# Kernel tuning notes

Measured on AMD Instinct MI355X. Metric: run time of the kernel, lower is better.

## Reference

```python
import jax, jax.numpy as jnp
import numpy as np

B = 524288
N_BUNDLES = 8
BUNDLE_DIM = 16
TOTAL_DIM = N_BUNDLES * BUNDLE_DIM  # 128
HIDDEN = 64
EPS = 1e-8


def setup_inputs() -> dict:
    key = jax.random.key(0)
    ks = jax.random.split(key, 8)
    z = jax.random.normal(ks[0], (B, TOTAL_DIM), dtype=jnp.float32)
    # norm MLP: Linear(n_bundles->hidden), GELU, Linear(hidden->hidden), GELU, Linear(hidden->n_bundles, no bias)
    W1 = jax.random.normal(ks[1], (HIDDEN, N_BUNDLES), dtype=jnp.float32) * (1.0 / np.sqrt(N_BUNDLES))
    b1 = jax.random.normal(ks[2], (HIDDEN,), dtype=jnp.float32) * 0.01
    W2 = jax.random.normal(ks[3], (HIDDEN, HIDDEN), dtype=jnp.float32) * (1.0 / np.sqrt(HIDDEN))
    b2 = jax.random.normal(ks[4], (HIDDEN,), dtype=jnp.float32) * 0.01
    W3 = jax.random.normal(ks[5], (N_BUNDLES, HIDDEN), dtype=jnp.float32) * (1.0 / np.sqrt(HIDDEN))
    # mixing_weights[i][j]: [d_i, d_j], init randn*0.01 -> stacked [n, n, d, d]
    mixW = jax.random.normal(ks[6], (N_BUNDLES, N_BUNDLES, BUNDLE_DIM, BUNDLE_DIM), dtype=jnp.float32) * 0.01
    gate_bias = jnp.zeros((N_BUNDLES,), dtype=jnp.float32)
    return {"z": z, "W1": W1, "b1": b1, "W2": W2, "b2": b2, "W3": W3,
            "mixW": mixW, "gate_bias": gate_bias}


def reference(z, W1, b1, W2, b2, W3, mixW, gate_bias):
    Bsz = z.shape[0]
    zb = z.reshape(Bsz, N_BUNDLES, BUNDLE_DIM)            # [B, n, d]
    # per-bundle norms (+eps as in torch source)
    norms = jnp.linalg.norm(zb, axis=-1) + EPS            # [B, n]
    # norm MLP with exact GELU (torch default), softplus scale
    h = jax.nn.gelu(norms @ W1.T + b1, approximate=False)
    h = jax.nn.gelu(h @ W2.T + b2, approximate=False)
    scales = jax.nn.softplus(h @ W3.T)                    # [B, n]
    equiv = zb * scales[:, :, None]                       # [B, n, d]
    # mixed_i = sum_j bundles_j @ W_ij^T ; mixW[i,j] is [d_out_i, d_in_j]
    mixed = jnp.einsum('bjk,ijdk->bid', zb, mixW)         # [B, n, d]
    gates = jax.nn.sigmoid(gate_bias)                     # [n]
    combined = equiv + gates[None, :, None] * mixed       # [B, n, d]
    return z + combined.reshape(Bsz, TOTAL_DIM)
```

## Files before the change

### kernel.cpp

```cpp
#include <hip/hip_runtime.h>
#include <hip/hip_bf16.h>

constexpr int NB  = 8;
constexpr int TD  = 128;
constexpr int HID = 64;
constexpr int ROWS = 128;

typedef __attribute__((ext_vector_type(8))) short bf16x8;
typedef __attribute__((ext_vector_type(4))) float f32x4;

union U { unsigned u[4]; bf16x8 v; };

__device__ __forceinline__ unsigned int pk2(float a, float b) {
    __hip_bfloat162 h = __float22bfloat162_rn(float2{a, b});
    unsigned int u; __builtin_memcpy(&u, &h, 4); return u;
}

__device__ __forceinline__ float gelu_fast(float x) {
    const float u = x * 0.70710678118f;
    const float a = fabsf(u);
    const float t = __builtin_amdgcn_rcpf(fmaf(0.3275911f, a, 1.0f));
    float p = fmaf(t, 1.061405429f, -1.453152027f);
    p = fmaf(t, p, 1.421413741f);
    p = fmaf(t, p, -0.284496736f);
    p = fmaf(t, p, 0.254829592f);
    p = p * t;
    const float e  = __builtin_amdgcn_exp2f(-a * a * 1.44269504f);
    const float pe = p * e;
    const float s  = (u >= 0.f) ? (2.0f - pe) : pe;
    return 0.5f * x * s;
}

constexpr size_t WS_NEED_BYTES = 10752 * 4;

__global__ __launch_bounds__(256, 1)
void cvt_weights(const float* __restrict__ W1, const float* __restrict__ W2,
                 const float* __restrict__ W3, const float* __restrict__ mixW,
                 unsigned* __restrict__ ws)
{
    const int t = threadIdx.x;
#pragma unroll
    for (int i = 0; i < 32; ++i) {
        const int p = t + i * 256;
        const int o = 2 * p;
        const int c = o >> 7, f = o & 127;
        const int ii = c >> 4, d = c & 15, j = f >> 4, k = f & 15;
        const float2 v = *(const float2*)(mixW + ii * 2048 + j * 256 + d * 16 + k);
        ws[p] = pk2(v.x, v.y);
    }
#pragma unroll
    for (int i = 0; i < 8; ++i) {
        const int p = t + i * 256;
        const float2 v = *(const float2*)(W2 + 2 * p);
        ws[8192 + p] = pk2(v.x, v.y);
    }
    {
        const float2 v1 = *(const float2*)(W1 + 2 * t);
        ws[10240 + t] = pk2(v1.x, v1.y);
        const float2 v3 = *(const float2*)(W3 + 2 * t);
        ws[10496 + t] = pk2(v3.x, v3.y);
    }
}

template<bool USE_WS>
__global__ __launch_bounds__(256, 4)
void soft_equiv(const float* __restrict__ z,  const float* __restrict__ W1,
                const float* __restrict__ b1, const float* __restrict__ W2,
                const float* __restrict__ b2, const float* __restrict__ W3,
                const float* __restrict__ mixW, const float* __restrict__ gb,
                const unsigned short* __restrict__ wsu,
                float* __restrict__ out)
{
    __shared__ __align__(16) unsigned short zs[ROWS * TD];
    __shared__ __align__(16) unsigned short hn[ROWS * NB];
    __shared__ float sca[ROWS * 9];

    const int t    = threadIdx.x;
    const int lane = t & 63;
    const int w    = t >> 6;
    const int hi   = lane >> 4;
    const int lo   = lane & 15;
    const size_t row0 = (size_t)blockIdx.x * ROWS;
    const float* ztile = z + row0 * TD;
    const f32x4 z4 = {0.f, 0.f, 0.f, 0.f};

    bf16x8 a1f[4];
    bf16x8 a2f[4][2];
    bf16x8 a3f[2];
    if constexpr (USE_WS) {
#pragma unroll
        for (int mt = 0; mt < 4; ++mt) {
            U c = {};
            if (hi == 0) c.v = *(const bf16x8*)(wsu + 2 * 10240 + (mt * 16 + lo) * 8);
            a1f[mt] = c.v;
        }
#pragma unroll
        for (int mt = 0; mt < 4; ++mt)
#pragma unroll
            for (int kk = 0; kk < 2; ++kk)
                a2f[mt][kk] = *(const bf16x8*)(wsu + 2 * 8192 + (mt * 16 + lo) * HID + kk * 32 + hi * 8);
#pragma unroll
        for (int kk = 0; kk < 2; ++kk) {
            U c = {};
            if (lo < NB) c.v = *(const bf16x8*)(wsu + 2 * 10496 + lo * HID + kk * 32 + hi * 8);
            a3f[kk] = c.v;
        }
    } else {
#pragma unroll
        for (int mt = 0; mt < 4; ++mt) {
            U c = {};
            if (hi == 0) {
                const float4 x = *(const float4*)(W1 + (mt * 16 + lo) * NB);
                const float4 y = *(const float4*)(W1 + (mt * 16 + lo) * NB + 4);
                c.u[0] = pk2(x.x, x.y); c.u[1] = pk2(x.z, x.w);
                c.u[2] = pk2(y.x, y.y); c.u[3] = pk2(y.z, y.w);
            }
            a1f[mt] = c.v;
        }
#pragma unroll
        for (int mt = 0; mt < 4; ++mt)
#pragma unroll
            for (int kk = 0; kk < 2; ++kk) {
                const float* p = W2 + (mt * 16 + lo) * HID + kk * 32 + hi * 8;
                const float4 x = *(const float4*)p;
                const float4 y = *(const float4*)(p + 4);
                U c;
                c.u[0] = pk2(x.x, x.y); c.u[1] = pk2(x.z, x.w);
                c.u[2] = pk2(y.x, y.y); c.u[3] = pk2(y.z, y.w);
                a2f[mt][kk] = c.v;
            }
#pragma unroll
        for (int kk = 0; kk < 2; ++kk) {
            U c = {};
            if (lo < NB) {
                const float* p = W3 + lo * HID + kk * 32 + hi * 8;
                const float4 x = *(const float4*)p;
                const float4 y = *(const float4*)(p + 4);
                c.u[0] = pk2(x.x, x.y); c.u[1] = pk2(x.z, x.w);
                c.u[2] = pk2(y.x, y.y); c.u[3] = pk2(y.z, y.w);
            }
            a3f[kk] = c.v;
        }
    }
    float4 b1v[4], b2v[4];
#pragma unroll
    for (int mt = 0; mt < 4; ++mt) {
        b1v[mt] = ((const float4*)b1)[mt * 4 + hi];
        b2v[mt] = ((const float4*)b2)[mt * 4 + hi];
    }

#pragma unroll
    for (int i = 0; i < 4; ++i) {
        const int r = 32 * w + i * 8 + (lane >> 3);
        const int b = lane & 7;
        const float* p = ztile + r * TD + b * 16;
        const float4 v0 = *(const float4*)(p);
        const float4 v1 = *(const float4*)(p + 4);
        const float4 v2 = *(const float4*)(p + 8);
        const float4 v3 = *(const float4*)(p + 12);
        const int sw = r & 7;
        uint4 q0 = { pk2(v0.x, v0.y), pk2(v0.z, v0.w), pk2(v1.x, v1.y), pk2(v1.z, v1.w) };
        uint4 q1 = { pk2(v2.x, v2.y), pk2(v2.z, v2.w), pk2(v3.x, v3.y), pk2(v3.z, v3.w) };
        *(uint4*)&zs[r * TD + (((2 * b    ) ^ sw) * 8)] = q0;
        *(uint4*)&zs[r * TD + (((2 * b + 1) ^ sw) * 8)] = q1;
        float s0 = 0.f, s1 = 0.f, s2 = 0.f, s3 = 0.f;
        s0 = fmaf(v0.x, v0.x, s0); s1 = fmaf(v0.y, v0.y, s1);
        s2 = fmaf(v0.z, v0.z, s2); s3 = fmaf(v0.w, v0.w, s3);
        s0 = fmaf(v1.x, v1.x, s0); s1 = fmaf(v1.y, v1.y, s1);
        s2 = fmaf(v1.z, v1.z, s2); s3 = fmaf(v1.w, v1.w, s3);
        s0 = fmaf(v2.x, v2.x, s0); s1 = fmaf(v2.y, v2.y, s1);
        s2 = fmaf(v2.z, v2.z, s2); s3 = fmaf(v2.w, v2.w, s3);
        s0 = fmaf(v3.x, v3.x, s0); s1 = fmaf(v3.y, v3.y, s1);
        s2 = fmaf(v3.z, v3.z, s2); s3 = fmaf(v3.w, v3.w, s3);
        const float nr = sqrtf((s0 + s1) + (s2 + s3)) + 1e-8f;
        __hip_bfloat16 hb = __float2bfloat16(nr);
        unsigned short us; __builtin_memcpy(&us, &hb, 2);
        hn[r * NB + b] = us;
    }

    bf16x8 b1f[2];
#pragma unroll
    for (int nt = 0; nt < 2; ++nt) {
        U c = {};
        if (hi == 0)
            c.v = *(const bf16x8*)&hn[(32 * w + nt * 16 + lo) * NB];
        b1f[nt] = c.v;
    }

    const int slA = lo + 32 * (hi & 1);
    const int slB = slA + 16;
    const bool selhi = (hi & 2) != 0;

    unsigned pkh[2][4][2];
#pragma unroll
    for (int nt = 0; nt < 2; ++nt)
#pragma unroll
        for (int mt = 0; mt < 4; ++mt) {
            f32x4 c = __builtin_amdgcn_mfma_f32_16x16x32_bf16(a1f[mt], b1f[nt], z4, 0, 0, 0);
            const float4 bb = b1v[mt];
            const float g0 = gelu_fast(c[0] + bb.x);
            const float g1 = gelu_fast(c[1] + bb.y);
            const float g2 = gelu_fast(c[2] + bb.z);
            const float g3 = gelu_fast(c[3] + bb.w);
            pkh[nt][mt][0] = pk2(g0, g1);
            pkh[nt][mt][1] = pk2(g2, g3);
        }

    bf16x8 b2f[2][2];
#pragma unroll
    for (int nt = 0; nt < 2; ++nt)
#pragma unroll
        for (int kk = 0; kk < 2; ++kk) {
            U c;
            const unsigned a0 = __shfl((int)pkh[nt][2*kk  ][0], slA, 64);
            const unsigned a1 = __shfl((int)pkh[nt][2*kk  ][1], slA, 64);
            const unsigned a2 = __shfl((int)pkh[nt][2*kk  ][0], slB, 64);
            const unsigned a3 = __shfl((int)pkh[nt][2*kk  ][1], slB, 64);
            const unsigned d0 = __shfl((int)pkh[nt][2*kk+1][0], slA, 64);
            const unsigned d1 = __shfl((int)pkh[nt][2*kk+1][1], slA, 64);
            const unsigned d2 = __shfl((int)pkh[nt][2*kk+1][0], slB, 64);
            const unsigned d3 = __shfl((int)pkh[nt][2*kk+1][1], slB, 64);
            c.u[0] = selhi ? d0 : a0; c.u[1] = selhi ? d1 : a1;
            c.u[2] = selhi ? d2 : a2; c.u[3] = selhi ? d3 : a3;
            b2f[nt][kk] = c.v;
        }

    unsigned pkh2[2][4][2];
#pragma unroll
    for (int nt = 0; nt < 2; ++nt)
#pragma unroll
        for (int mt = 0; mt < 4; ++mt) {
            f32x4 c = __builtin_amdgcn_mfma_f32_16x16x32_bf16(a2f[mt][0], b2f[nt][0], z4, 0, 0, 0);
            c = __builtin_amdgcn_mfma_f32_16x16x32_bf16(a2f[mt][1], b2f[nt][1], c, 0, 0, 0);
            const float4 bb = b2v[mt];
            const float g0 = gelu_fast(c[0] + bb.x);
            const float g1 = gelu_fast(c[1] + bb.y);
            const float g2 = gelu_fast(c[2] + bb.z);
            const float g3 = gelu_fast(c[3] + bb.w);
            pkh2[nt][mt][0] = pk2(g0, g1);
            pkh2[nt][mt][1] = pk2(g2, g3);
        }

#pragma unroll
    for (int nt = 0; nt < 2; ++nt) {
        U c0, c1;
#pragma unroll
        for (int kk = 0; kk < 2; ++kk) {
            const unsigned a0 = __shfl((int)pkh2[nt][2*kk  ][0], slA, 64);
            const unsigned a1 = __shfl((int)pkh2[nt][2*kk  ][1], slA, 64);
            const unsigned a2 = __shfl((int)pkh2[nt][2*kk  ][0], slB, 64);
            const unsigned a3 = __shfl((int)pkh2[nt][2*kk  ][1], slB, 64);
            const unsigned d0 = __shfl((int)pkh2[nt][2*kk+1][0], slA, 64);
            const unsigned d1 = __shfl((int)pkh2[nt][2*kk+1][1], slA, 64);
            const unsigned d2 = __shfl((int)pkh2[nt][2*kk+1][0], slB, 64);
            const unsigned d3 = __shfl((int)pkh2[nt][2*kk+1][1], slB, 64);
            if (kk == 0) {
                c0.u[0] = selhi ? d0 : a0; c0.u[1] = selhi ? d1 : a1;
                c0.u[2] = selhi ? d2 : a2; c0.u[3] = selhi ? d3 : a3;
            } else {
                c1.u[0] = selhi ? d0 : a0; c1.u[1] = selhi ? d1 : a1;
                c1.u[2] = selhi ? d2 : a2; c1.u[3] = selhi ? d3 : a3;
            }
        }
        f32x4 s3 = __builtin_amdgcn_mfma_f32_16x16x32_bf16(a3f[0], c0.v, z4, 0, 0, 0);
        s3 = __builtin_amdgcn_mfma_f32_16x16x32_bf16(a3f[1], c1.v, s3, 0, 0, 0);
        if (hi < 2) {
            const int r = 32 * w + nt * 16 + lo;
#pragma unroll
            for (int e = 0; e < 4; ++e) {
                const float x  = s3[e];
                const float sp = fmaxf(x, 0.f) +
                    0.69314718f * __builtin_amdgcn_logf(
                        1.0f + __builtin_amdgcn_exp2f(-fabsf(x) * 1.44269504f));
                sca[r * 9 + hi * 4 + e] = 1.0f + sp;
            }
        }
    }

    bf16x8 bfr[2][4];
#pragma unroll
    for (int n = 0; n < 2; ++n) {
        const int col = w * 32 + n * 16 + lo;
#pragma unroll
        for (int kk = 0; kk < 4; ++kk) {
            if constexpr (USE_WS) {
                bfr[n][kk] = *(const bf16x8*)(wsu + col * TD + kk * 32 + hi * 8);
            } else {
                const int k0 = kk * 32 + hi * 8;
                const float* p = mixW + (col >> 4) * 2048 + (k0 >> 4) * 256
                                      + (col & 15) * 16 + (k0 & 15);
                const float4 x = *(const float4*)p;
                const float4 y = *(const float4*)(p + 4);
                U c;
                c.u[0] = pk2(x.x, x.y); c.u[1] = pk2(x.z, x.w);
                c.u[2] = pk2(y.x, y.y); c.u[3] = pk2(y.z, y.w);
                bfr[n][kk] = c.v;
            }
        }
    }
    const float g0 = 1.f / (1.f + __builtin_amdgcn_exp2f(-gb[2 * w + 0] * 1.44269504f));
    const float g1 = 1.f / (1.f + __builtin_amdgcn_exp2f(-gb[2 * w + 1] * 1.44269504f));

    __syncthreads();

#pragma unroll
    for (int m = 0; m < 8; ++m) {
        const int ar = m * 16 + lo;
        bf16x8 af[4];
#pragma unroll
        for (int kk = 0; kk < 4; ++kk) {
            const int slot = (kk * 4 + hi) ^ (ar & 7);
            af[kk] = *(const bf16x8*)&zs[ar * TD + slot * 8];
        }
        f32x4 acc0 = z4, acc1 = z4;
#pragma unroll
        for (int kk = 0; kk < 4; ++kk)
            acc0 = __builtin_amdgcn_mfma_f32_16x16x32_bf16(af[kk], bfr[0][kk], acc0, 0, 0, 0);
#pragma unroll
        for (int kk = 0; kk < 4; ++kk)
            acc1 = __builtin_amdgcn_mfma_f32_16x16x32_bf16(af[kk], bfr[1][kk], acc1, 0, 0, 0);

        const int col0 = w * 32 + lo;
        const int col1 = col0 + 16;
        const int sl0 = col0 >> 3, cw0 = col0 & 7;
        const int sl1 = col1 >> 3, cw1 = col1 & 7;
#pragma unroll
        for (int e = 0; e < 4; ++e) {
            const int rr = m * 16 + hi * 4 + e;
            const int swr = rr & 7;
            const float sc0 = sca[rr * 9 + 2 * w + 0];
            const float sc1 = sca[rr * 9 + 2 * w + 1];
            const float zv0 = __uint_as_float(
                (unsigned int)zs[rr * TD + ((sl0 ^ swr) * 8) + cw0] << 16);
            const float zv1 = __uint_as_float(
                (unsigned int)zs[rr * TD + ((sl1 ^ swr) * 8) + cw1] << 16);
            float* orow = &out[(row0 + rr) * TD];
            __builtin_nontemporal_store(fmaf(zv0, sc0, g0 * acc0[e]), orow + col0);
            __builtin_nontemporal_store(fmaf(zv1, sc1, g1 * acc1[e]), orow + col1);
        }
    }
}

extern "C" void kernel_launch(void* const* d_in, const int* in_sizes, int n_in,
                              void* d_out, int out_size, void* d_ws, size_t ws_size,
                              hipStream_t stream) {
    const float* z    = (const float*)d_in[0];
    const float* W1   = (const float*)d_in[1];
    const float* b1   = (const float*)d_in[2];
    const float* W2   = (const float*)d_in[3];
    const float* b2   = (const float*)d_in[4];
    const float* W3   = (const float*)d_in[5];
    const float* mixW = (const float*)d_in[6];
    const float* gb   = (const float*)d_in[7];
    float* out = (float*)d_out;

    const int B = in_sizes[0] / TD;
    if (ws_size >= WS_NEED_BYTES && d_ws != nullptr) {
        cvt_weights<<<1, 256, 0, stream>>>(W1, W2, W3, mixW, (unsigned*)d_ws);
        soft_equiv<true><<<B / ROWS, 256, 0, stream>>>(
            z, W1, b1, W2, b2, W3, mixW, gb, (const unsigned short*)d_ws, out);
    } else {
        soft_equiv<false><<<B / ROWS, 256, 0, stream>>>(
            z, W1, b1, W2, b2, W3, mixW, gb, nullptr, out);
    }
}
```

Before: 110.1 us.

## Repartition mixing GEMM so each wave owns its rows and drop block barrier

The mixing GEMM epilogue is re-partitioned so each wave processes its own 32 rows across all 128 output columns instead of 32 columns across all rows. This lets the A fragments come from rows the same wave produced and removes the __syncthreads before the GEMM. In exchange each wave loads four times as many B (mixW) fragments inside the loop and all eight gate values are computed per thread, adding memory traffic and register pressure.

```diff
diff --git a/kernel.cpp b/kernel.cpp
--- a/kernel.cpp
+++ b/kernel.cpp
@@ -277,66 +277,85 @@
         }
     }
 
-    bf16x8 bfr[2][4];
-#pragma unroll
-    for (int n = 0; n < 2; ++n) {
-        const int col = w * 32 + n * 16 + lo;
+    const float gg[8] = {
+        1.f / (1.f + __builtin_amdgcn_exp2f(-gb[0] * 1.44269504f)),
+        1.f / (1.f + __builtin_amdgcn_exp2f(-gb[1] * 1.44269504f)),
+        1.f / (1.f + __builtin_amdgcn_exp2f(-gb[2] * 1.44269504f)),
+        1.f / (1.f + __builtin_amdgcn_exp2f(-gb[3] * 1.44269504f)),
+        1.f / (1.f + __builtin_amdgcn_exp2f(-gb[4] * 1.44269504f)),
+        1.f / (1.f + __builtin_amdgcn_exp2f(-gb[5] * 1.44269504f)),
+        1.f / (1.f + __builtin_amdgcn_exp2f(-gb[6] * 1.44269504f)),
+        1.f / (1.f + __builtin_amdgcn_exp2f(-gb[7] * 1.44269504f)) };
+
+    bf16x8 af[2][4];
+#pragma unroll
+    for (int mt = 0; mt < 2; ++mt) {
+        const int ar = 32 * w + mt * 16 + lo;
+#pragma unroll
+        for (int kk = 0; kk < 4; ++kk) {
+            const int slot = (kk * 4 + hi) ^ (ar & 7);
+            af[mt][kk] = *(const bf16x8*)&zs[ar * TD + slot * 8];
+        }
+    }
+
+#pragma unroll
+    for (int np = 0; np < 4; ++np) {
+        bf16x8 bf0[4], bf1[4];
+        const int col0 = np * 32 + lo;
+        const int col1 = col0 + 16;
 #pragma unroll
         for (int kk = 0; kk < 4; ++kk) {
             if constexpr (USE_WS) {
-                bfr[n][kk] = *(const bf16x8*)(wsu + col * TD + kk * 32 + hi * 8);
+                bf0[kk] = *(const bf16x8*)(wsu + col0 * TD + kk * 32 + hi * 8);
+                bf1[kk] = *(const bf16x8*)(wsu + col1 * TD + kk * 32 + hi * 8);
             } else {
                 const int k0 = kk * 32 + hi * 8;
-                const float* p = mixW + (col >> 4) * 2048 + (k0 >> 4) * 256
-                                      + (col & 15) * 16 + (k0 & 15);
-                const float4 x = *(const float4*)p;
-                const float4 y = *(const float4*)(p + 4);
+                const float* p0 = mixW + (col0 >> 4) * 2048 + (k0 >> 4) * 256
+                                       + (col0 & 15) * 16 + (k0 & 15);
+                const float* p1 = mixW + (col1 >> 4) * 2048 + (k0 >> 4) * 256
+                                       + (col1 & 15) * 16 + (k0 & 15);
+                const float4 x0 = *(const float4*)p0;
+                const float4 y0 = *(const float4*)(p0 + 4);
+                const float4 x1 = *(const float4*)p1;
+                const float4 y1 = *(const float4*)(p1 + 4);
                 U c;
-                c.u[0] = pk2(x.x, x.y); c.u[1] = pk2(x.z, x.w);
-                c.u[2] = pk2(y.x, y.y); c.u[3] = pk2(y.z, y.w);
-                bfr[n][kk] = c.v;
-            }
-        }
-    }
-    const float g0 = 1.f / (1.f + __builtin_amdgcn_exp2f(-gb[2 * w + 0] * 1.44269504f));
-    const float g1 = 1.f / (1.f + __builtin_amdgcn_exp2f(-gb[2 * w + 1] * 1.44269504f));
-
-    __syncthreads();
-
-#pragma unroll
-    for (int m = 0; m < 8; ++m) {
-        const int ar = m * 16 + lo;
-        bf16x8 af[4];
-#pragma unroll
-        for (int kk = 0; kk < 4; ++kk) {
-            const int slot = (kk * 4 + hi) ^ (ar & 7);
-            af[kk] = *(const bf16x8*)&zs[ar * TD + slot * 8];
-        }
-        f32x4 acc0 = z4, acc1 = z4;
-#pragma unroll
-        for (int kk = 0; kk < 4; ++kk)
-            acc0 = __builtin_amdgcn_mfma_f32_16x16x32_bf16(af[kk], bfr[0][kk], acc0, 0, 0, 0);
-#pragma unroll
-        for (int kk = 0; kk < 4; ++kk)
-            acc1 = __builtin_amdgcn_mfma_f32_16x16x32_bf16(af[kk], bfr[1][kk], acc1, 0, 0, 0);
-
-        const int col0 = w * 32 + lo;
-        const int col1 = col0 + 16;
+                c.u[0] = pk2(x0.x, x0.y); c.u[1] = pk2(x0.z, x0.w);
+                c.u[2] = pk2(y0.x, y0.y); c.u[3] = pk2(y0.z, y0.w);
+                bf0[kk] = c.v;
+                c.u[0] = pk2(x1.x, x1.y); c.u[1] = pk2(x1.z, x1.w);
+                c.u[2] = pk2(y1.x, y1.y); c.u[3] = pk2(y1.z, y1.w);
+                bf1[kk] = c.v;
+            }
+        }
+        const float g0 = gg[np * 2 + 0];
+        const float g1 = gg[np * 2 + 1];
         const int sl0 = col0 >> 3, cw0 = col0 & 7;
         const int sl1 = col1 >> 3, cw1 = col1 & 7;
-#pragma unroll
-        for (int e = 0; e < 4; ++e) {
-            const int rr = m * 16 + hi * 4 + e;
-            const int swr = rr & 7;
-            const float sc0 = sca[rr * 9 + 2 * w + 0];
-            const float sc1 = sca[rr * 9 + 2 * w + 1];
-            const float zv0 = __uint_as_float(
-                (unsigned int)zs[rr * TD + ((sl0 ^ swr) * 8) + cw0] << 16);
-            const float zv1 = __uint_as_float(
-                (unsigned int)zs[rr * TD + ((sl1 ^ swr) * 8) + cw1] << 16);
-            float* orow = &out[(row0 + rr) * TD];
-            __builtin_nontemporal_store(fmaf(zv0, sc0, g0 * acc0[e]), orow + col0);
-            __builtin_nontemporal_store(fmaf(zv1, sc1, g1 * acc1[e]), orow + col1);
+
+#pragma unroll
+        for (int mt = 0; mt < 2; ++mt) {
+            f32x4 acc0 = z4, acc1 = z4;
+#pragma unroll
+            for (int kk = 0; kk < 4; ++kk)
+                acc0 = __builtin_amdgcn_mfma_f32_16x16x32_bf16(af[mt][kk], bf0[kk], acc0, 0, 0, 0);
+#pragma unroll
+            for (int kk = 0; kk < 4; ++kk)
+                acc1 = __builtin_amdgcn_mfma_f32_16x16x32_bf16(af[mt][kk], bf1[kk], acc1, 0, 0, 0);
+
+#pragma unroll
+            for (int e = 0; e < 4; ++e) {
+                const int rr = 32 * w + mt * 16 + hi * 4 + e;
+                const int swr = rr & 7;
+                const float sc0 = sca[rr * 9 + np * 2 + 0];
+                const float sc1 = sca[rr * 9 + np * 2 + 1];
+                const float zv0 = __uint_as_float(
+                    (unsigned int)zs[rr * TD + ((sl0 ^ swr) * 8) + cw0] << 16);
+                const float zv1 = __uint_as_float(
+                    (unsigned int)zs[rr * TD + ((sl1 ^ swr) * 8) + cw1] << 16);
+                float* orow = &out[(row0 + rr) * TD];
+                __builtin_nontemporal_store(fmaf(zv0, sc0, g0 * acc0[e]), orow + col0);
+                __builtin_nontemporal_store(fmaf(zv1, sc1, g1 * acc1[e]), orow + col1);
+            }
         }
     }
 }
```

Result: slower. 175.6 us (+59.5%).
